# Kernel optimization log

Measured on AMD Instinct MI355X. Metric: run time of the kernel, lower is better.

Reference implementation:

```python
import jax, jax.numpy as jnp
import numpy as np


def _log_exp_kernel(x):
    # positive feature map log(1 + exp(x)) (softplus), per the kernel's name
    return jax.nn.softplus(x)


def setup_inputs() -> dict:
    key0 = jax.random.key(0)
    ks = jax.random.split(key0, 8)
    N, L, H, d = 2, 2048, 8, 64
    D = H * d
    s = 1.0 / np.sqrt(D)
    return {
        "query": jax.random.normal(ks[0], (N, L, D), jnp.float32),
        "key": jax.random.normal(ks[1], (N, L, D), jnp.float32),
        "Wq": jax.random.normal(ks[2], (D, D), jnp.float32) * s,
        "Wk": jax.random.normal(ks[3], (D, D), jnp.float32) * s,
        "Wv": jax.random.normal(ks[4], (D, D), jnp.float32) * s,
        "position_coeffs": jax.random.normal(ks[5], (H, d), jnp.float32),
        "position_weight": jax.random.normal(ks[6], (H, d, 1), jnp.float32) * 0.02,
        "position_bias": jax.random.normal(ks[7], (H, d), jnp.float32) * 0.02,
    }


def reference(query, key, Wq, Wk, Wv, position_coeffs, position_weight, position_bias):
    N, Lq, D = query.shape
    Lk = key.shape[1]
    H, d, P = position_weight.shape

    # default positions: arange, P=1 (broadcast over batch)
    qpos = jnp.arange(Lq, dtype=query.dtype).reshape(1, Lq, 1)  # (1, Lq, P)

    # projections + kernel feature map; (N, H, L, d)
    q = _log_exp_kernel((query @ Wq.T).reshape(N, Lq, H, d)).transpose(0, 2, 1, 3)
    k = _log_exp_kernel((key @ Wk.T).reshape(N, Lk, H, d)).transpose(0, 2, 1, 3)
    v = (key @ Wv.T).reshape(N, Lk, H, d).transpose(0, 2, 1, 3)

    # projected positions; NOTE: source uses query_positions for pk too (faithful)
    pq = jnp.einsum('nlp,hkp->nhlk', qpos, position_weight) + position_bias[None, :, None, :]
    pk = jnp.einsum('nlp,hkp->nhlk', qpos, position_weight)  # (1, H, Lq, d)

    coeff = position_coeffs[None, :, None, :]  # (1, H, 1, d)
    cos_a = q * jnp.cos(pq)
    cos_b = coeff * k * jnp.cos(pk)
    sin_a = q * jnp.sin(pq)
    sin_b = coeff * k * jnp.sin(pk)

    # (N, H, Lq, Lk) quadratic score
    score = (jnp.einsum('nhqd,nhkd->nhqk', cos_a, cos_b)
             + jnp.einsum('nhqd,nhkd->nhqk', sin_a, sin_b))

    # future mask (future_offset = 0): zero out keys j > query i
    future = jnp.arange(Lk)[None, :] > jnp.arange(Lq)[:, None]
    score = jnp.where(future[None, None], jnp.zeros((), score.dtype), score)

    # scaled: rows sum (in abs) to 1
    score = score / jnp.sum(jnp.abs(score), axis=-1, keepdims=True)

    att = jnp.einsum('nhqk,nhkd->nhqd', score, v)
    return att.transpose(0, 2, 1, 3).reshape(N, Lq, D)
```

## Files before the change

kernel.cpp:

```cpp
#include <hip/hip_runtime.h>
#include <hip/hip_bf16.h>
#include <cstdint>


typedef __bf16 bf16x8 __attribute__((ext_vector_type(8)));
typedef float f32x16 __attribute__((ext_vector_type(16)));
typedef unsigned short u16x8 __attribute__((ext_vector_type(8)));
typedef uint32_t u32x4 __attribute__((ext_vector_type(4)));

__device__ __forceinline__ unsigned short f2bfu(float f) {
    uint32_t u = __float_as_uint(f);
    uint32_t r = (u + 0x7fffu + ((u >> 16) & 1u)) >> 16;
    return (unsigned short)r;
}
__device__ __forceinline__ uint32_t cvt2(float a, float b) {
    __hip_bfloat162 h = __float22bfloat162_rn(make_float2(a, b));
    return *reinterpret_cast<uint32_t*>(&h);
}
__device__ __forceinline__ float softplusf(float x) {
    return fmaxf(x, 0.f) + __logf(1.f + __expf(-fabsf(x)));
}
__device__ __forceinline__ uint32_t pkbf(float a, float b) {
    uint32_t d;
    asm("v_cvt_pk_bf16_f32 %0, %1, %2" : "=v"(d) : "v"(a), "v"(b));
    return d;
}
__device__ __forceinline__ void plswap(uint32_t& a, uint32_t& b) {
    asm volatile("v_permlane32_swap_b32 %0, %1" : "+v"(a), "+v"(b));
}
__device__ __forceinline__ void gload16(const unsigned short* g, unsigned short* l) {
    __builtin_amdgcn_global_load_lds(
        (const __attribute__((address_space(1))) unsigned int*)g,
        (__attribute__((address_space(3))) unsigned int*)l, 16, 0, 0);
}

__global__ __launch_bounds__(256) void cvt_kernel(
    const float* __restrict__ query, const float* __restrict__ key,
    const float* __restrict__ Wq, const float* __restrict__ Wk,
    const float* __restrict__ Wv,
    unsigned short* __restrict__ Xqb, unsigned short* __restrict__ Xkb,
    unsigned short* __restrict__ Wqb, unsigned short* __restrict__ Wkb,
    unsigned short* __restrict__ Wvb)
{
    const int z = blockIdx.z;
    const float* src;
    unsigned short* dst;
    int n8;
    if (z == 0)      { src = query; dst = Xqb; n8 = 4096 * 512 / 8; }
    else if (z == 1) { src = key;   dst = Xkb; n8 = 4096 * 512 / 8; }
    else if (z == 2) { src = Wq;    dst = Wqb; n8 = 512 * 512 / 8;  }
    else if (z == 3) { src = Wk;    dst = Wkb; n8 = 512 * 512 / 8;  }
    else             { src = Wv;    dst = Wvb; n8 = 512 * 512 / 8;  }
    int idx = blockIdx.x * 256 + threadIdx.x;
    if (idx >= n8) return;
    const float4* s = (const float4*)src + (size_t)idx * 2;
    float4 a = s[0], b = s[1];
    uint4 o;
    o.x = cvt2(a.x, a.y); o.y = cvt2(a.z, a.w);
    o.z = cvt2(b.x, b.y); o.w = cvt2(b.z, b.w);
    *(uint4*)&dst[(size_t)idx * 8] = o;
}

#define XTILE (128 * 64)
#define WTILE (64 * 64)

__global__ __launch_bounds__(256) void proj_kernel(
    const unsigned short* __restrict__ Xqb, const unsigned short* __restrict__ Xkb,
    const unsigned short* __restrict__ Wqb, const unsigned short* __restrict__ Wkb,
    const unsigned short* __restrict__ Wvb, const float* __restrict__ coef,
    const float* __restrict__ posw, const float* __restrict__ posb,
    unsigned short* __restrict__ Af, unsigned short* __restrict__ Bf,
    unsigned short* __restrict__ Vf)
{
    const int mode = blockIdx.z;
    const int c0 = blockIdx.x * 64;
    const int m0 = blockIdx.y * 128;
    const unsigned short* X = (mode == 0) ? Xqb : Xkb;
    const unsigned short* W = (mode == 0) ? Wqb : (mode == 1 ? Wkb : Wvb);

    __shared__ __align__(16) unsigned short smem[2 * XTILE + 2 * WTILE];

    const int t = threadIdx.x;
    const int lane = t & 63, wv = t >> 6;
    const int lm = lane & 31, half = lane >> 5;
    const int wrow = wv >> 1, wcol = wv & 1;

    f32x16 acc[2] = {};

    auto stage = [&](int kt, int b) {
        int ko = kt * 64;
        unsigned short* xd = smem + b * XTILE;
        unsigned short* wd = smem + 2 * XTILE + b * WTILE;
#pragma unroll
        for (int it = 0; it < 4; ++it) {
            int cid = t + it * 256, row = cid >> 3, seg = cid & 7;
            const unsigned short* src =
                X + (size_t)(m0 + row) * 512 + ko + (((seg ^ (row & 7)) << 3));
            gload16(src, xd + cid * 8);
        }
#pragma unroll
        for (int it = 0; it < 2; ++it) {
            int cid = t + it * 256, row = cid >> 3, seg = cid & 7;
            const unsigned short* src =
                W + (size_t)(c0 + row) * 512 + ko + (((seg ^ (row & 7)) << 3));
            gload16(src, wd + cid * 8);
        }
    };

    stage(0, 0);
    const int rx = 64 * wrow + lm, rw = 32 * wcol + lm;
    for (int kt = 0; kt < 8; ++kt) {
        if (kt < 7) {
            stage(kt + 1, (kt + 1) & 1);
            asm volatile("s_waitcnt vmcnt(6)" ::: "memory");
        } else {
            asm volatile("s_waitcnt vmcnt(0)" ::: "memory");
        }
        __builtin_amdgcn_s_barrier();

        const unsigned short* xb = smem + (kt & 1) * XTILE;
        const unsigned short* wb = smem + 2 * XTILE + (kt & 1) * WTILE;
        __builtin_amdgcn_s_setprio(1);
#pragma unroll
        for (int ks = 0; ks < 4; ++ks) {
            int sA = (((half + 2 * ks) ^ (lm & 7)) << 3);
            bf16x8 a0 = *(const bf16x8*)&xb[rx * 64 + sA];
            bf16x8 a1 = *(const bf16x8*)&xb[(rx + 32) * 64 + sA];
            bf16x8 b  = *(const bf16x8*)&wb[rw * 64 + sA];
            acc[0] = __builtin_amdgcn_mfma_f32_32x32x16_bf16(a0, b, acc[0], 0, 0, 0);
            acc[1] = __builtin_amdgcn_mfma_f32_32x32x16_bf16(a1, b, acc[1], 0, 0, 0);
        }
        __builtin_amdgcn_s_setprio(0);
        asm volatile("s_waitcnt lgkmcnt(0)" ::: "memory");
        __builtin_amdgcn_sched_barrier(0);
        __builtin_amdgcn_s_barrier();
    }

    if (mode != 2) {
        unsigned short* Feat = (mode == 0) ? Af : Bf;
        int c = c0 + 32 * wcol + lm;
        int h = c >> 6, jj = c & 63;
        float wgt = posw[c];
        float bia = (mode == 0) ? posb[c] : 0.f;
        float cf  = (mode == 1) ? coef[c] : 1.f;
#pragma unroll
        for (int i = 0; i < 2; ++i)
#pragma unroll
        for (int r = 0; r < 16; ++r) {
            int rl = (r & 3) + 8 * (r >> 2) + 4 * half;
            int m = m0 + 64 * wrow + 32 * i + rl;
            int n = m >> 11, l = m & 2047;
            float ang = (float)l * wgt + bia;
            float sn, cs; __sincosf(ang, &sn, &cs);
            float v = softplusf(acc[i][r]) * cf;
            size_t base = ((size_t)(n * 8 + h) * 2048 + l) * 128 + jj;
            Feat[base]      = f2bfu(v * cs);
            Feat[base + 64] = f2bfu(v * sn);
        }
    } else {
        float* tb = (float*)smem;
        float* tbw = tb + wv * (32 * 34);
        __syncthreads();
#pragma unroll
        for (int i = 0; i < 2; ++i) {
#pragma unroll
            for (int r = 0; r < 16; ++r) {
                int rl = (r & 3) + 8 * (r >> 2) + 4 * half;
                tbw[lm * 34 + rl] = acc[i][r];
            }
            int mb = m0 + 64 * wrow + 32 * i;
            int n = mb >> 11, l0 = mb & 2047;
#pragma unroll
            for (int rep = 0; rep < 16; ++rep) {
                int cl = rep * 2 + half;
                float v = tbw[cl * 34 + lm];
                int c = c0 + 32 * wcol + cl;
                int h = c >> 6, dd = c & 63;
                Vf[((size_t)(n * 8 + h) * 64 + dd) * 2048 + l0 + lm] = f2bfu(v);
            }
        }
    }
}

__global__ __launch_bounds__(256) void attn_kernel(
    const unsigned short* __restrict__ Af, const unsigned short* __restrict__ Bf,
    const unsigned short* __restrict__ Vf, float* __restrict__ out)
{
    const int bx = blockIdx.x;
    const int nh = bx & 15;
    const int p  = bx >> 4;
    const int qq = (p < 16) ? p : 47 - p;
    const int q0 = qq * 64;

    __shared__ unsigned short Bs[64 * 136];
    __shared__ unsigned short Vs[64 * 72];
    __shared__ float zf[64];

    const int t = threadIdx.x;
    const int lane = t & 63, wv = t >> 6;
    const int lm = lane & 31, half = lane >> 5;
    const int qb = wv >> 1, kb = wv & 1;
    const int n = nh >> 3, h = nh & 7;

    const unsigned short* Ah = Af + (size_t)nh * 2048 * 128;
    const unsigned short* Bh = Bf + (size_t)nh * 2048 * 128;
    const unsigned short* Vh = Vf + (size_t)nh * 64 * 2048;

#pragma unroll
    for (int it = 0; it < 4; ++it) {
        int cid = t + it * 256, row = cid >> 4, off = (cid & 15) << 3;
        *(u16x8*)&Bs[row * 136 + off] = *(const u16x8*)&Ah[(size_t)(q0 + row) * 128 + off];
    }
    if (t < 64) zf[t] = 0.f;
    __syncthreads();
    bf16x8 qfrag[8];
    {
        const unsigned short* ab = &Bs[(32 * qb + lm) * 136 + half * 8];
#pragma unroll
        for (int c = 0; c < 8; ++c) qfrag[c] = *(const bf16x8*)(ab + c * 16);
    }

    f32x16 oacc0 = {}, oacc1 = {};
    float zsum = 0.f;

    u16x8 pb[4], pv[2];
#pragma unroll
    for (int it = 0; it < 4; ++it) {
        int cid = t + it * 256, row = cid >> 4, off = (cid & 15) << 3;
        pb[it] = *(const u16x8*)&Bh[(size_t)row * 128 + off];
    }
#pragma unroll
    for (int it = 0; it < 2; ++it) {
        int cid = t + it * 256, row = cid >> 3, off = (cid & 7) << 3;
        pv[it] = *(const u16x8*)&Vh[(size_t)row * 2048 + off];
    }

    for (int kt = 0; kt <= qq; ++kt) {
        __syncthreads();
#pragma unroll
        for (int it = 0; it < 4; ++it) {
            int cid = t + it * 256, row = cid >> 4, off = (cid & 15) << 3;
            *(u16x8*)&Bs[row * 136 + off] = pb[it];
        }
#pragma unroll
        for (int it = 0; it < 2; ++it) {
            int cid = t + it * 256, row = cid >> 3, off = (cid & 7) << 3;
            *(u16x8*)&Vs[row * 72 + off] = pv[it];
        }
        __syncthreads();
        if (kt < qq) {
            int k1 = (kt + 1) * 64;
#pragma unroll
            for (int it = 0; it < 4; ++it) {
                int cid = t + it * 256, row = cid >> 4, off = (cid & 15) << 3;
                pb[it] = *(const u16x8*)&Bh[(size_t)(k1 + row) * 128 + off];
            }
#pragma unroll
            for (int it = 0; it < 2; ++it) {
                int cid = t + it * 256, row = cid >> 3, off = (cid & 7) << 3;
                pv[it] = *(const u16x8*)&Vh[(size_t)row * 2048 + k1 + off];
            }
        }

        f32x16 sacc = {};
        const unsigned short* kbase = &Bs[(32 * kb + lm) * 136 + half * 8];
        __builtin_amdgcn_s_setprio(1);
#pragma unroll
        for (int ks = 0; ks < 8; ++ks) {
            bf16x8 kf = *(const bf16x8*)(kbase + ks * 16);
            sacc = __builtin_amdgcn_mfma_f32_32x32x16_bf16(kf, qfrag[ks], sacc, 0, 0, 0);
        }
        __builtin_amdgcn_s_setprio(0);

        if (kt == qq) {
#pragma unroll
            for (int r = 0; r < 16; ++r) {
                int kl = (r & 3) + 8 * (r >> 2) + 4 * half;
                if ((32 * kb + kl) > (32 * qb + lm)) sacc[r] = 0.f;
            }
        }
#pragma unroll
        for (int r = 0; r < 16; ++r) zsum += fabsf(sacc[r]);

        union { u32x4 u; bf16x8 b; } pa0, pa1;
        {
            uint32_t A = pkbf(sacc[0], sacc[1]);
            uint32_t B = pkbf(sacc[2], sacc[3]);
            uint32_t C = pkbf(sacc[4], sacc[5]);
            uint32_t D = pkbf(sacc[6], sacc[7]);
            plswap(A, C);
            plswap(B, D);
            pa0.u = (u32x4){A, B, C, D};
            uint32_t E = pkbf(sacc[8], sacc[9]);
            uint32_t F = pkbf(sacc[10], sacc[11]);
            uint32_t G = pkbf(sacc[12], sacc[13]);
            uint32_t H = pkbf(sacc[14], sacc[15]);
            plswap(E, G);
            plswap(F, H);
            pa1.u = (u32x4){E, F, G, H};
        }

        const unsigned short* v0 = &Vs[(size_t)lm * 72 + 32 * kb + half * 8];
        const unsigned short* v1 = &Vs[(size_t)(32 + lm) * 72 + 32 * kb + half * 8];
        __builtin_amdgcn_s_setprio(1);
        {
            bf16x8 vb00 = *(const bf16x8*)(v0);
            bf16x8 vb10 = *(const bf16x8*)(v1);
            oacc0 = __builtin_amdgcn_mfma_f32_32x32x16_bf16(pa0.b, vb00, oacc0, 0, 0, 0);
            oacc1 = __builtin_amdgcn_mfma_f32_32x32x16_bf16(pa0.b, vb10, oacc1, 0, 0, 0);
            bf16x8 vb01 = *(const bf16x8*)(v0 + 16);
            bf16x8 vb11 = *(const bf16x8*)(v1 + 16);
            oacc0 = __builtin_amdgcn_mfma_f32_32x32x16_bf16(pa1.b, vb01, oacc0, 0, 0, 0);
            oacc1 = __builtin_amdgcn_mfma_f32_32x32x16_bf16(pa1.b, vb11, oacc1, 0, 0, 0);
        }
        __builtin_amdgcn_s_setprio(0);
    }

    atomicAdd(&zf[32 * qb + lm], zsum);
    __syncthreads();

    float* Os = (float*)Bs;
    if (kb == 0) {
#pragma unroll
        for (int r = 0; r < 16; ++r) {
            int ql = (r & 3) + 8 * (r >> 2) + 4 * half;
            Os[(32 * qb + ql) * 65 + lm]      = oacc0[r];
            Os[(32 * qb + ql) * 65 + 32 + lm] = oacc1[r];
        }
    }
    __syncthreads();
    if (kb == 1) {
#pragma unroll
        for (int r = 0; r < 16; ++r) {
            int ql = (r & 3) + 8 * (r >> 2) + 4 * half;
            int q = q0 + 32 * qb + ql;
            float invz = 1.f / zf[32 * qb + ql];
            float o0 = (Os[(32 * qb + ql) * 65 + lm]      + oacc0[r]) * invz;
            float o1 = (Os[(32 * qb + ql) * 65 + 32 + lm] + oacc1[r]) * invz;
            size_t base = ((size_t)(n * 2048 + q)) * 512 + h * 64;
            out[base + lm]      = o0;
            out[base + 32 + lm] = o1;
        }
    }
}

extern "C" void kernel_launch(void* const* d_in, const int* in_sizes, int n_in,
                              void* d_out, int out_size, void* d_ws, size_t ws_size,
                              hipStream_t stream) {
    (void)in_sizes; (void)n_in; (void)out_size; (void)ws_size;
    const float* query = (const float*)d_in[0];
    const float* key   = (const float*)d_in[1];
    const float* Wq    = (const float*)d_in[2];
    const float* Wk    = (const float*)d_in[3];
    const float* Wv    = (const float*)d_in[4];
    const float* coef  = (const float*)d_in[5];
    const float* posw  = (const float*)d_in[6];
    const float* posb  = (const float*)d_in[7];

    unsigned short* Af  = (unsigned short*)d_ws;
    unsigned short* Bf  = Af + (size_t)16 * 2048 * 128;
    unsigned short* Vf  = Bf + (size_t)16 * 2048 * 128;
    unsigned short* Xqb = Vf + (size_t)16 * 64 * 2048;
    unsigned short* Xkb = Xqb + (size_t)4096 * 512;
    unsigned short* Wqb = Xkb + (size_t)4096 * 512;
    unsigned short* Wkb = Wqb + (size_t)512 * 512;
    unsigned short* Wvb = Wkb + (size_t)512 * 512;

    cvt_kernel<<<dim3(1024, 1, 5), 256, 0, stream>>>(
        query, key, Wq, Wk, Wv, Xqb, Xkb, Wqb, Wkb, Wvb);
    proj_kernel<<<dim3(8, 32, 3), 256, 0, stream>>>(
        Xqb, Xkb, Wqb, Wkb, Wvb, coef, posw, posb, Af, Bf, Vf);
    attn_kernel<<<dim3(512), 256, 0, stream>>>(
        Af, Bf, Vf, (float*)d_out);
}
```

Baseline: 130.0 us.

## Split causal key tiles by parity across blocks with 128-row query tiles

The attention kernel now gives each block two 64-row query tiles that share every staged key/value tile, doubling reuse of each shared-memory load. Key tiles are split by even/odd parity between two blocks, which writes partial outputs and partial row-abs-sums. A new normalisation kernel adds the two partials and divides by the summed norms. The proj grid axes are also swapped to change block ordering. The cost is an extra kernel launch and a full fp32 output round-trip through global memory.

```diff
diff --git a/kernel.cpp b/kernel.cpp
--- a/kernel.cpp
+++ b/kernel.cpp
@@ -73,8 +73,8 @@
     unsigned short* __restrict__ Vf)
 {
     const int mode = blockIdx.z;
-    const int c0 = blockIdx.x * 64;
-    const int m0 = blockIdx.y * 128;
+    const int m0 = blockIdx.x * 128;
+    const int c0 = blockIdx.y * 64;
     const unsigned short* X = (mode == 0) ? Xqb : Xkb;
     const unsigned short* W = (mode == 0) ? Wqb : (mode == 1 ? Wkb : Wvb);
 
@@ -184,17 +184,22 @@
 
 __global__ __launch_bounds__(256) void attn_kernel(
     const unsigned short* __restrict__ Af, const unsigned short* __restrict__ Bf,
-    const unsigned short* __restrict__ Vf, float* __restrict__ out)
+    const unsigned short* __restrict__ Vf, float* __restrict__ out,
+    float* __restrict__ opart, float* __restrict__ z0, float* __restrict__ z1)
 {
-    const int bx = blockIdx.x;
-    const int nh = bx & 15;
-    const int p  = bx >> 4;
-    const int qq = (p < 16) ? p : 47 - p;
-    const int q0 = qq * 64;
+    const int bid = blockIdx.x;
+    const int parity = bid >> 8;
+    const int rr = bid & 255;
+    const int nh = rr & 15;
+    const int jraw = rr >> 4;
+    const int j = parity ? (15 - jraw) : jraw;
+    const int q0 = j * 128;
+    const int kmaxA = 2 * j;
+    const int kmaxB = 2 * j + 1;
 
     __shared__ unsigned short Bs[64 * 136];
     __shared__ unsigned short Vs[64 * 72];
-    __shared__ float zf[64];
+    __shared__ float zf[128];
 
     const int t = threadIdx.x;
     const int lane = t & 63, wv = t >> 6;
@@ -206,36 +211,37 @@
     const unsigned short* Bh = Bf + (size_t)nh * 2048 * 128;
     const unsigned short* Vh = Vf + (size_t)nh * 64 * 2048;
 
-#pragma unroll
-    for (int it = 0; it < 4; ++it) {
-        int cid = t + it * 256, row = cid >> 4, off = (cid & 15) << 3;
-        *(u16x8*)&Bs[row * 136 + off] = *(const u16x8*)&Ah[(size_t)(q0 + row) * 128 + off];
-    }
-    if (t < 64) zf[t] = 0.f;
-    __syncthreads();
-    bf16x8 qfrag[8];
+    bf16x8 qfA[8], qfB[8];
     {
-        const unsigned short* ab = &Bs[(32 * qb + lm) * 136 + half * 8];
-#pragma unroll
-        for (int c = 0; c < 8; ++c) qfrag[c] = *(const bf16x8*)(ab + c * 16);
-    }
-
-    f32x16 oacc0 = {}, oacc1 = {};
-    float zsum = 0.f;
+        const unsigned short* qra = &Ah[(size_t)(q0 + 32 * qb + lm) * 128 + half * 8];
+        const unsigned short* qrb = qra + (size_t)64 * 128;
+#pragma unroll
+        for (int c = 0; c < 8; ++c) {
+            qfA[c] = *(const bf16x8*)(qra + c * 16);
+            qfB[c] = *(const bf16x8*)(qrb + c * 16);
+        }
+    }
+    if (t < 128) zf[t] = 0.f;
+
+    f32x16 oA0 = {}, oA1 = {}, oB0 = {}, oB1 = {};
+    float zA = 0.f, zB = 0.f;
 
     u16x8 pb[4], pv[2];
-#pragma unroll
-    for (int it = 0; it < 4; ++it) {
-        int cid = t + it * 256, row = cid >> 4, off = (cid & 15) << 3;
-        pb[it] = *(const u16x8*)&Bh[(size_t)row * 128 + off];
-    }
-#pragma unroll
-    for (int it = 0; it < 2; ++it) {
-        int cid = t + it * 256, row = cid >> 3, off = (cid & 7) << 3;
-        pv[it] = *(const u16x8*)&Vh[(size_t)row * 2048 + off];
-    }
-
-    for (int kt = 0; kt <= qq; ++kt) {
+    {
+        const int k0 = parity * 64;
+#pragma unroll
+        for (int it = 0; it < 4; ++it) {
+            int cid = t + it * 256, row = cid >> 4, off = (cid & 15) << 3;
+            pb[it] = *(const u16x8*)&Bh[(size_t)(k0 + row) * 128 + off];
+        }
+#pragma unroll
+        for (int it = 0; it < 2; ++it) {
+            int cid = t + it * 256, row = cid >> 3, off = (cid & 7) << 3;
+            pv[it] = *(const u16x8*)&Vh[(size_t)row * 2048 + k0 + off];
+        }
+    }
+
+    for (int kt = parity; kt <= kmaxB; kt += 2) {
         __syncthreads();
 #pragma unroll
         for (int it = 0; it < 4; ++it) {
@@ -248,8 +254,8 @@
             *(u16x8*)&Vs[row * 72 + off] = pv[it];
         }
         __syncthreads();
-        if (kt < qq) {
-            int k1 = (kt + 1) * 64;
+        if (kt + 2 <= kmaxB) {
+            int k1 = (kt + 2) * 64;
 #pragma unroll
             for (int it = 0; it < 4; ++it) {
                 int cid = t + it * 256, row = cid >> 4, off = (cid & 15) << 3;
@@ -262,70 +268,98 @@
             }
         }
 
-        f32x16 sacc = {};
+        const bool doA = (kt <= kmaxA);
+        f32x16 sA = {}, sB = {};
         const unsigned short* kbase = &Bs[(32 * kb + lm) * 136 + half * 8];
         __builtin_amdgcn_s_setprio(1);
 #pragma unroll
         for (int ks = 0; ks < 8; ++ks) {
             bf16x8 kf = *(const bf16x8*)(kbase + ks * 16);
-            sacc = __builtin_amdgcn_mfma_f32_32x32x16_bf16(kf, qfrag[ks], sacc, 0, 0, 0);
+            if (doA) sA = __builtin_amdgcn_mfma_f32_32x32x16_bf16(kf, qfA[ks], sA, 0, 0, 0);
+            sB = __builtin_amdgcn_mfma_f32_32x32x16_bf16(kf, qfB[ks], sB, 0, 0, 0);
         }
         __builtin_amdgcn_s_setprio(0);
-
-        if (kt == qq) {
-#pragma unroll
-            for (int r = 0; r < 16; ++r) {
-                int kl = (r & 3) + 8 * (r >> 2) + 4 * half;
-                if ((32 * kb + kl) > (32 * qb + lm)) sacc[r] = 0.f;
-            }
-        }
-#pragma unroll
-        for (int r = 0; r < 16; ++r) zsum += fabsf(sacc[r]);
-
-        union { u32x4 u; bf16x8 b; } pa0, pa1;
-        {
-            uint32_t A = pkbf(sacc[0], sacc[1]);
-            uint32_t B = pkbf(sacc[2], sacc[3]);
-            uint32_t C = pkbf(sacc[4], sacc[5]);
-            uint32_t D = pkbf(sacc[6], sacc[7]);
-            plswap(A, C);
-            plswap(B, D);
-            pa0.u = (u32x4){A, B, C, D};
-            uint32_t E = pkbf(sacc[8], sacc[9]);
-            uint32_t F = pkbf(sacc[10], sacc[11]);
-            uint32_t G = pkbf(sacc[12], sacc[13]);
-            uint32_t H = pkbf(sacc[14], sacc[15]);
-            plswap(E, G);
-            plswap(F, H);
-            pa1.u = (u32x4){E, F, G, H};
-        }
 
         const unsigned short* v0 = &Vs[(size_t)lm * 72 + 32 * kb + half * 8];
         const unsigned short* v1 = &Vs[(size_t)(32 + lm) * 72 + 32 * kb + half * 8];
-        __builtin_amdgcn_s_setprio(1);
+        bf16x8 vb00 = *(const bf16x8*)(v0);
+        bf16x8 vb10 = *(const bf16x8*)(v1);
+        bf16x8 vb01 = *(const bf16x8*)(v0 + 16);
+        bf16x8 vb11 = *(const bf16x8*)(v1 + 16);
+
+        if (doA) {
+            if (kt == kmaxA) {
+#pragma unroll
+                for (int r = 0; r < 16; ++r) {
+                    int kl = (r & 3) + 8 * (r >> 2) + 4 * half;
+                    if ((32 * kb + kl) > (32 * qb + lm)) sA[r] = 0.f;
+                }
+            }
+#pragma unroll
+            for (int r = 0; r < 16; ++r) zA += fabsf(sA[r]);
+            union { u32x4 u; bf16x8 b; } pa0, pa1;
+            {
+                uint32_t A = pkbf(sA[0], sA[1]),  B = pkbf(sA[2], sA[3]);
+                uint32_t C = pkbf(sA[4], sA[5]),  D = pkbf(sA[6], sA[7]);
+                plswap(A, C); plswap(B, D);
+                pa0.u = (u32x4){A, B, C, D};
+                uint32_t E = pkbf(sA[8], sA[9]),  F = pkbf(sA[10], sA[11]);
+                uint32_t G = pkbf(sA[12], sA[13]), H = pkbf(sA[14], sA[15]);
+                plswap(E, G); plswap(F, H);
+                pa1.u = (u32x4){E, F, G, H};
+            }
+            __builtin_amdgcn_s_setprio(1);
+            oA0 = __builtin_amdgcn_mfma_f32_32x32x16_bf16(pa0.b, vb00, oA0, 0, 0, 0);
+            oA1 = __builtin_amdgcn_mfma_f32_32x32x16_bf16(pa0.b, vb10, oA1, 0, 0, 0);
+            oA0 = __builtin_amdgcn_mfma_f32_32x32x16_bf16(pa1.b, vb01, oA0, 0, 0, 0);
+            oA1 = __builtin_amdgcn_mfma_f32_32x32x16_bf16(pa1.b, vb11, oA1, 0, 0, 0);
+            __builtin_amdgcn_s_setprio(0);
+        }
         {
-            bf16x8 vb00 = *(const bf16x8*)(v0);
-            bf16x8 vb10 = *(const bf16x8*)(v1);
-            oacc0 = __builtin_amdgcn_mfma_f32_32x32x16_bf16(pa0.b, vb00, oacc0, 0, 0, 0);
-            oacc1 = __builtin_amdgcn_mfma_f32_32x32x16_bf16(pa0.b, vb10, oacc1, 0, 0, 0);
-            bf16x8 vb01 = *(const bf16x8*)(v0 + 16);
-            bf16x8 vb11 = *(const bf16x8*)(v1 + 16);
-            oacc0 = __builtin_amdgcn_mfma_f32_32x32x16_bf16(pa1.b, vb01, oacc0, 0, 0, 0);
-            oacc1 = __builtin_amdgcn_mfma_f32_32x32x16_bf16(pa1.b, vb11, oacc1, 0, 0, 0);
-        }
-        __builtin_amdgcn_s_setprio(0);
-    }
-
-    atomicAdd(&zf[32 * qb + lm], zsum);
+            if (kt == kmaxB) {
+#pragma unroll
+                for (int r = 0; r < 16; ++r) {
+                    int kl = (r & 3) + 8 * (r >> 2) + 4 * half;
+                    if ((32 * kb + kl) > (32 * qb + lm)) sB[r] = 0.f;
+                }
+            }
+#pragma unroll
+            for (int r = 0; r < 16; ++r) zB += fabsf(sB[r]);
+            union { u32x4 u; bf16x8 b; } pb0, pb1;
+            {
+                uint32_t A = pkbf(sB[0], sB[1]),  B = pkbf(sB[2], sB[3]);
+                uint32_t C = pkbf(sB[4], sB[5]),  D = pkbf(sB[6], sB[7]);
+                plswap(A, C); plswap(B, D);
+                pb0.u = (u32x4){A, B, C, D};
+                uint32_t E = pkbf(sB[8], sB[9]),  F = pkbf(sB[10], sB[11]);
+                uint32_t G = pkbf(sB[12], sB[13]), H = pkbf(sB[14], sB[15]);
+                plswap(E, G); plswap(F, H);
+                pb1.u = (u32x4){E, F, G, H};
+            }
+            __builtin_amdgcn_s_setprio(1);
+            oB0 = __builtin_amdgcn_mfma_f32_32x32x16_bf16(pb0.b, vb00, oB0, 0, 0, 0);
+            oB1 = __builtin_amdgcn_mfma_f32_32x32x16_bf16(pb0.b, vb10, oB1, 0, 0, 0);
+            oB0 = __builtin_amdgcn_mfma_f32_32x32x16_bf16(pb1.b, vb01, oB0, 0, 0, 0);
+            oB1 = __builtin_amdgcn_mfma_f32_32x32x16_bf16(pb1.b, vb11, oB1, 0, 0, 0);
+            __builtin_amdgcn_s_setprio(0);
+        }
+    }
+
+    atomicAdd(&zf[32 * qb + lm], zA);
+    atomicAdd(&zf[64 + 32 * qb + lm], zB);
     __syncthreads();
 
+    float* zdst = parity ? z1 : z0;
+    if (t < 128) zdst[(size_t)nh * 2048 + q0 + t] = zf[t];
+
+    float* dst = parity ? opart : out;
     float* Os = (float*)Bs;
     if (kb == 0) {
 #pragma unroll
         for (int r = 0; r < 16; ++r) {
             int ql = (r & 3) + 8 * (r >> 2) + 4 * half;
-            Os[(32 * qb + ql) * 65 + lm]      = oacc0[r];
-            Os[(32 * qb + ql) * 65 + 32 + lm] = oacc1[r];
+            Os[(32 * qb + ql) * 65 + lm]      = oA0[r];
+            Os[(32 * qb + ql) * 65 + 32 + lm] = oA1[r];
         }
     }
     __syncthreads();
@@ -334,14 +368,53 @@
         for (int r = 0; r < 16; ++r) {
             int ql = (r & 3) + 8 * (r >> 2) + 4 * half;
             int q = q0 + 32 * qb + ql;
-            float invz = 1.f / zf[32 * qb + ql];
-            float o0 = (Os[(32 * qb + ql) * 65 + lm]      + oacc0[r]) * invz;
-            float o1 = (Os[(32 * qb + ql) * 65 + 32 + lm] + oacc1[r]) * invz;
             size_t base = ((size_t)(n * 2048 + q)) * 512 + h * 64;
-            out[base + lm]      = o0;
-            out[base + 32 + lm] = o1;
-        }
-    }
+            dst[base + lm]      = Os[(32 * qb + ql) * 65 + lm]      + oA0[r];
+            dst[base + 32 + lm] = Os[(32 * qb + ql) * 65 + 32 + lm] + oA1[r];
+        }
+    }
+    __syncthreads();
+    if (kb == 0) {
+#pragma unroll
+        for (int r = 0; r < 16; ++r) {
+            int ql = (r & 3) + 8 * (r >> 2) + 4 * half;
+            Os[(32 * qb + ql) * 65 + lm]      = oB0[r];
+            Os[(32 * qb + ql) * 65 + 32 + lm] = oB1[r];
+        }
+    }
+    __syncthreads();
+    if (kb == 1) {
+#pragma unroll
+        for (int r = 0; r < 16; ++r) {
+            int ql = (r & 3) + 8 * (r >> 2) + 4 * half;
+            int q = q0 + 64 + 32 * qb + ql;
+            size_t base = ((size_t)(n * 2048 + q)) * 512 + h * 64;
+            dst[base + lm]      = Os[(32 * qb + ql) * 65 + lm]      + oB0[r];
+            dst[base + 32 + lm] = Os[(32 * qb + ql) * 65 + 32 + lm] + oB1[r];
+        }
+    }
+}
+
+__global__ __launch_bounds__(256) void norm_kernel(
+    const float* __restrict__ opart, const float* __restrict__ z0,
+    const float* __restrict__ z1, float* __restrict__ out)
+{
+    int idx = blockIdx.x * 256 + threadIdx.x;
+    int i = idx << 2;
+    int row = i >> 9;
+    int c = i & 511;
+    int n = row >> 11, q = row & 2047;
+    int h = c >> 6;
+    size_t zi = (size_t)(n * 8 + h) * 2048 + q;
+    float rz = 1.f / (z0[zi] + z1[zi]);
+    float4 o = *(const float4*)&out[i];
+    float4 pp = *(const float4*)&opart[i];
+    float4 r;
+    r.x = (o.x + pp.x) * rz;
+    r.y = (o.y + pp.y) * rz;
+    r.z = (o.z + pp.z) * rz;
+    r.w = (o.w + pp.w) * rz;
+    *(float4*)&out[i] = r;
 }
 
 extern "C" void kernel_launch(void* const* d_in, const int* in_sizes, int n_in,
@@ -365,11 +438,16 @@
     unsigned short* Wqb = Xkb + (size_t)4096 * 512;
     unsigned short* Wkb = Wqb + (size_t)512 * 512;
     unsigned short* Wvb = Wkb + (size_t)512 * 512;
+    float* opart = (float*)(Wvb + (size_t)512 * 512);
+    float* z0    = opart + (size_t)2 * 2048 * 512;
+    float* z1    = z0 + (size_t)16 * 2048;
 
     cvt_kernel<<<dim3(1024, 1, 5), 256, 0, stream>>>(
         query, key, Wq, Wk, Wv, Xqb, Xkb, Wqb, Wkb, Wvb);
-    proj_kernel<<<dim3(8, 32, 3), 256, 0, stream>>>(
+    proj_kernel<<<dim3(32, 8, 3), 256, 0, stream>>>(
         Xqb, Xkb, Wqb, Wkb, Wvb, coef, posw, posb, Af, Bf, Vf);
     attn_kernel<<<dim3(512), 256, 0, stream>>>(
-        Af, Bf, Vf, (float*)d_out);
-}
+        Af, Bf, Vf, (float*)d_out, opart, z0, z1);
+    norm_kernel<<<dim3(2048), 256, 0, stream>>>(
+        opart, z0, z1, (float*)d_out);
+}
```

New measurement: 129.1 us. No clear change (-0.7%).
